# Kernel optimization log

Hardware: AMD Instinct MI355X
Metric: run time of the kernel (lower is better)

Reference implementation:

```python
import jax, jax.numpy as jnp
import numpy as np

B, N, D, DM, K = 2, 768, 32, 64, 16


def _linparams(key, cin, cout):
    kw, kb, ks, kt = jax.random.split(key, 4)
    W = jax.random.normal(kw, (cin, cout), jnp.float32) * np.float32(1.0 / np.sqrt(cin))
    b = 0.01 * jax.random.normal(kb, (cout,), jnp.float32)
    s = jax.random.uniform(ks, (cout,), jnp.float32, 0.5, 1.5)  # folded BN scale
    t = 0.1 * jax.random.normal(kt, (cout,), jnp.float32)       # folded BN shift
    return W, b, s, t


def setup_inputs():
    key = jax.random.key(0)
    kx, kh, k0, k1, k2, k3, k4 = jax.random.split(key, 7)
    inp = {
        'x': jax.random.normal(kx, (B, N, 3), jnp.float32),
        'h': jax.random.normal(kh, (B, N, D), jnp.float32),
    }
    specs = [('e0', 2 * D + 1, DM), ('e1', DM, DM), ('c0', DM, DM), ('c1', DM, 1), ('n0', D + DM, D)]
    for (name, cin, cout), k in zip(specs, [k0, k1, k2, k3, k4]):
        W, b, s, t = _linparams(k, cin, cout)
        inp[name + 'W'], inp[name + 'b'], inp[name + 's'], inp[name + 't'] = W, b, s, t
    return inp


def _layer(f, W, b, s, t):
    # 1x1 conv (= linear over last dim) + BN folded to per-channel affine + ReLU
    return jax.nn.relu((f @ W + b) * s + t)


def reference(x, h, e0W, e0b, e0s, e0t, e1W, e1b, e1s, e1t,
              c0W, c0b, c0s, c0t, c1W, c1b, c1s, c1t,
              n0W, n0b, n0s, n0t):
    Bn, Nn, Dn = h.shape
    # x_center[b,i,j] = x[b,j]; x_neighbor[b,i,j] = x[b,i]  => diff = x_j - x_i
    x_diff = x[:, None, :, :] - x[:, :, None, :]                   # (B,N,N,3)
    d2 = jnp.sum(x_diff * x_diff, axis=-1, keepdims=True)          # (B,N,N,1)
    h_c = jnp.broadcast_to(h[:, None, :, :], (Bn, Nn, Nn, Dn))     # h_center
    h_n = jnp.broadcast_to(h[:, :, None, :], (Bn, Nn, Nn, Dn))     # h_neighbor
    edge_feat = jnp.concatenate([h_c, h_n, d2], axis=-1)           # (B,N,N,2D+1)
    m_edge = _layer(_layer(edge_feat, e0W, e0b, e0s, e0t), e1W, e1b, e1s, e1t)  # (B,N,N,DM)
    w = _layer(_layer(m_edge, c0W, c0b, c0s, c0t), c1W, c1b, c1s, c1t)          # (B,N,N,1)
    x_update = x + jnp.sum(w * x_diff, axis=2)                     # (B,N,3)
    # knn gather: k nearest neighbors (incl. self) by squared distance
    idx = jax.lax.top_k(-d2[..., 0], K)[1]                         # (B,N,K)
    m_gathered = jnp.take_along_axis(m_edge, idx[..., None], axis=2)  # (B,N,K,DM)
    m_node = jnp.sum(m_gathered, axis=2)                           # (B,N,DM)
    node_feat = jnp.concatenate([h, m_node], axis=-1)              # (B,N,D+DM)
    h_update = _layer(node_feat, n0W, n0b, n0s, n0t)               # (B,N,D)
    return (x_update, h_update)
```

## Files before the change

### kernel.cpp

```cpp
#include <hip/hip_runtime.h>
#include <hip/hip_bf16.h>

#define Bn  2
#define Nn  768
#define Dh  32
#define DMm 64
#define KK  16
#define GI  3
#define TPRE 256
#define TMAIN 512
#define SAB 176

typedef __bf16 bf16x8 __attribute__((ext_vector_type(8)));
typedef float  f32x4  __attribute__((ext_vector_type(4)));


__global__ __launch_bounds__(TPRE) void egnn_pre(
    const float* __restrict__ X,  const float* __restrict__ H,
    const float* __restrict__ e0W, const float* __restrict__ e0b,
    const float* __restrict__ e0s, const float* __restrict__ e0t,
    const float* __restrict__ e1W, const float* __restrict__ e1b,
    const float* __restrict__ e1s, const float* __restrict__ e1t,
    const float* __restrict__ c0W, const float* __restrict__ c0b,
    const float* __restrict__ c0s, const float* __restrict__ c0t,
    const float* __restrict__ c1W, const float* __restrict__ c1b,
    const float* __restrict__ c1s, const float* __restrict__ c1t,
    const float* __restrict__ n0W, const float* __restrict__ n0b,
    const float* __restrict__ n0s, const float* __restrict__ n0t,
    __bf16* __restrict__ G1, float* __restrict__ G2,
    __bf16* __restrict__ W1f, __bf16* __restrict__ W2Tf,
    float* __restrict__ o1v, float* __restrict__ o2w3,
    float* __restrict__ Wnf, float* __restrict__ onOff,
    float* __restrict__ wd2, float* __restrict__ misc,
    int* __restrict__ knnIdx)
{
    const int tid = threadIdx.x;
    if (blockIdx.x < 384) {
        const int lane = tid & 63;
        const int row_i = blockIdx.x * 4 + (tid >> 6);
        const int b = row_i / Nn;
        const float xi0 = X[(size_t)row_i * 3 + 0];
        const float xi1 = X[(size_t)row_i * 3 + 1];
        const float xi2 = X[(size_t)row_i * 3 + 2];
        float v[Nn / 64];
        #pragma unroll
        for (int k = 0; k < Nn / 64; ++k) {
            int j = lane + (k << 6);
            size_t rj = (size_t)(b * Nn + j) * 3;
            float dx = X[rj + 0] - xi0;
            float dy = X[rj + 1] - xi1;
            float dz = X[rj + 2] - xi2;
            v[k] = __fadd_rn(__fadd_rn(__fmul_rn(dx, dx), __fmul_rn(dy, dy)),
                             __fmul_rn(dz, dz));
        }
        for (int r = 0; r < KK; ++r) {
            float bv = 3.4e38f; int bidx = Nn;
            #pragma unroll
            for (int k = 0; k < Nn / 64; ++k)
                if (v[k] < bv) { bv = v[k]; bidx = lane + (k << 6); }
            #pragma unroll
            for (int off = 32; off >= 1; off >>= 1) {
                float ov = __shfl_down(bv, off);
                int   oi = __shfl_down(bidx, off);
                if (ov < bv || (ov == bv && oi < bidx)) { bv = ov; bidx = oi; }
            }
            bidx = __shfl(bidx, 0);
            if (lane == 0) knnIdx[row_i * KK + r] = bidx;
            if ((bidx & 63) == lane) v[bidx >> 6] = 3.4e38f;
        }
    } else if (blockIdx.x < 432) {
        __shared__ float sWa[Dh * DMm], sWb[Dh * DMm], sOff[DMm], sH[32 * Dh];
        for (int k = tid; k < Dh * DMm; k += TPRE) {
            float s = e0s[k & 63];
            sWa[k] = e0W[k] * s;
            sWb[k] = e0W[Dh * DMm + k] * s;
        }
        if (tid < DMm) sOff[tid] = fmaf(e0b[tid], e0s[tid], e0t[tid]);
        const int row0 = (blockIdx.x - 384) * 32;
        for (int k = tid; k < 32 * Dh; k += TPRE) sH[k] = H[(size_t)row0 * Dh + k];
        __syncthreads();

        const int r = tid >> 3, g = tid & 7;
        float g1[8], g2[8];
        #pragma unroll
        for (int e = 0; e < 8; ++e) { g1[e] = 0.f; g2[e] = sOff[g * 8 + e]; }
        #pragma unroll
        for (int d = 0; d < Dh; ++d) {
            float hv = sH[r * Dh + d];
            #pragma unroll
            for (int e = 0; e < 8; ++e) {
                g1[e] = fmaf(hv, sWa[d * DMm + g * 8 + e], g1[e]);
                g2[e] = fmaf(hv, sWb[d * DMm + g * 8 + e], g2[e]);
            }
        }
        const size_t row = row0 + r;
        bf16x8 o;
        #pragma unroll
        for (int e = 0; e < 8; ++e) o[e] = (__bf16)g1[e];
        *(bf16x8*)(G1 + row * DMm + g * 8) = o;
        *(float4*)(G2 + row * DMm + g * 8)     = make_float4(g2[0], g2[1], g2[2], g2[3]);
        *(float4*)(G2 + row * DMm + g * 8 + 4) = make_float4(g2[4], g2[5], g2[6], g2[7]);
    } else {
        for (int src = tid; src < 4096; src += TPRE) {
            int k = src >> 6, n = src & 63;
            int fi = ((((k >> 5) * 4 + (n >> 4)) * 64) + ((k >> 3) & 3) * 16 + (n & 15)) * 8 + (k & 7);
            W1f[fi]  = (__bf16)(e1W[src] * e1s[n]);
            W2Tf[fi] = (__bf16)(c0W[src] * c0s[n]);
        }
        if (tid < DMm) {
            o1v[tid] = fmaf(e1b[tid], e1s[tid], e1t[tid]);
            wd2[tid] = e0W[64 * DMm + tid] * e0s[tid];
        }
        for (int u = tid; u < 1024; u += TPRE) {
            int lane = u >> 4, rem = u & 15, t4 = rem >> 2, r = rem & 3;
            int ch = t4 * 16 + (lane >> 4) * 4 + r;
            o2w3[2 * u]     = fmaf(c0b[ch], c0s[ch], c0t[ch]);
            o2w3[2 * u + 1] = c1W[ch] * c1s[0];
        }
        for (int idx = tid; idx < (Dh + DMm) * Dh; idx += TPRE)
            Wnf[idx] = n0W[idx] * n0s[idx & 31];
        if (tid < Dh) onOff[tid] = fmaf(n0b[tid], n0s[tid], n0t[tid]);
        if (tid == 0) misc[0] = fmaf(c1b[0], c1s[0], c1t[0]);
    }
}

__global__ __launch_bounds__(TMAIN, 2) void egnn_main(
    const float* __restrict__ X,  const float* __restrict__ H,
    const __bf16* __restrict__ G1, const float* __restrict__ G2,
    const __bf16* __restrict__ W1f, const __bf16* __restrict__ W2Tf,
    const float* __restrict__ o1v, const float* __restrict__ o2w3,
    const float* __restrict__ Wnf, const float* __restrict__ onOff,
    const float* __restrict__ wd2, const float* __restrict__ misc,
    const int* __restrict__ knnIdx,
    float* __restrict__ out)
{
    const int bid = blockIdx.x;
    const int b  = bid >> 8;
    const int i0 = (bid & 255) * GI;
    const int tid = threadIdx.x;
    const int wv = tid >> 6;
    const int lane = tid & 63;
    const int l15 = lane & 15;
    const int q   = lane >> 4;

    __shared__ float  sX[Nn * 3];
    __shared__ float  sD2[GI * Nn];
    __shared__ float  sWj[GI * Nn];
    __shared__ char   sHit[GI * Nn];
    __shared__ float  sMnode[GI * DMm];
    __shared__ float  sFeat[GI * 96];
    __shared__ float  sXacc[GI * 3];
    __shared__ __align__(16) char sA1[8][16 * SAB];

    for (int k = tid; k < Nn * 3; k += TMAIN) sX[k] = X[(size_t)b * Nn * 3 + k];
    for (int k = tid; k < GI * Nn / 4; k += TMAIN) ((int*)sHit)[k] = 0;
    if (tid < GI * DMm) sMnode[tid] = 0.f;
    if (tid < GI * Dh) {
        int i_l = tid >> 5, c = tid & 31;
        sFeat[i_l * 96 + c] = H[(size_t)(b * Nn + i0 + i_l) * Dh + c];
    }
    __syncthreads();

    #pragma unroll
    for (int i_l = 0; i_l < GI; ++i_l) {
        float xi0 = sX[(i0 + i_l) * 3 + 0];
        float xi1 = sX[(i0 + i_l) * 3 + 1];
        float xi2 = sX[(i0 + i_l) * 3 + 2];
        for (int j = tid; j < Nn; j += TMAIN) {
            float dx = sX[j * 3 + 0] - xi0;
            float dy = sX[j * 3 + 1] - xi1;
            float dz = sX[j * 3 + 2] - xi2;
            sD2[i_l * Nn + j] = __fadd_rn(__fadd_rn(__fmul_rn(dx, dx), __fmul_rn(dy, dy)),
                                          __fmul_rn(dz, dz));
        }
    }
    if (tid < GI * KK) {
        int i_l = tid >> 4, r = tid & 15;
        int idx = knnIdx[(size_t)(b * Nn + i0 + i_l) * KK + r];
        sHit[i_l * Nn + idx] = 1;
    }

    bf16x8 w1f[2][4], w2f[2][4];
    #pragma unroll
    for (int s = 0; s < 2; ++s)
        #pragma unroll
        for (int t4 = 0; t4 < 4; ++t4) {
            w1f[s][t4] = *(const bf16x8*)(W1f + (((s * 4 + t4) * 64 + lane) << 3));
            w2f[s][t4] = *(const bf16x8*)(W2Tf + (((s * 4 + t4) * 64 + lane) << 3));
        }
    float wd2c[2][8];
    #pragma unroll
    for (int s = 0; s < 2; ++s) {
        const float4* wp = (const float4*)(wd2 + s * 32 + q * 8);
        float4 wa = wp[0], wc = wp[1];
        wd2c[s][0] = wa.x; wd2c[s][1] = wa.y; wd2c[s][2] = wa.z; wd2c[s][3] = wa.w;
        wd2c[s][4] = wc.x; wd2c[s][5] = wc.y; wd2c[s][6] = wc.z; wd2c[s][7] = wc.w;
    }
    float o1c[4];
    #pragma unroll
    for (int t4 = 0; t4 < 4; ++t4) o1c[t4] = o1v[t4 * 16 + l15];
    float4 o2w3q[8];
    #pragma unroll
    for (int u = 0; u < 8; ++u) o2w3q[u] = ((const float4*)o2w3)[lane * 8 + u];
    const float c1off = misc[0];
    __syncthreads();

    for (int i_l = 0; i_l < GI; ++i_l) {
        const int ig = i0 + i_l;
        float g2c[2][8];
        #pragma unroll
        for (int s = 0; s < 2; ++s) {
            const float4* gp = (const float4*)(G2 + (size_t)(b * Nn + ig) * DMm + s * 32 + q * 8);
            float4 ga = gp[0], gc = gp[1];
            g2c[s][0] = ga.x; g2c[s][1] = ga.y; g2c[s][2] = ga.z; g2c[s][3] = ga.w;
            g2c[s][4] = gc.x; g2c[s][5] = gc.y; g2c[s][6] = gc.z; g2c[s][7] = gc.w;
        }
        for (int t = wv; t < 48; t += 8) {
            const int base = t * 16;
            const int jm = base + l15;

            float d2v = sD2[i_l * Nn + jm];

            bf16x8 a0f[2];
            #pragma unroll
            for (int s = 0; s < 2; ++s) {
                bf16x8 g1v = *(const bf16x8*)(G1 + (size_t)(b * Nn + jm) * DMm + s * 32 + q * 8);
                bf16x8 af;
                #pragma unroll
                for (int e = 0; e < 8; ++e) {
                    float v = fmaf(d2v, wd2c[s][e], g2c[s][e]) + (float)g1v[e];
                    af[e] = (__bf16)fmaxf(v, 0.f);
                }
                a0f[s] = af;
            }

            f32x4 acc[4];
            #pragma unroll
            for (int t4 = 0; t4 < 4; ++t4) acc[t4] = f32x4{0.f, 0.f, 0.f, 0.f};
            #pragma unroll
            for (int s = 0; s < 2; ++s)
                #pragma unroll
                for (int t4 = 0; t4 < 4; ++t4)
                    acc[t4] = __builtin_amdgcn_mfma_f32_16x16x32_bf16(a0f[s], w1f[s][t4], acc[t4], 0, 0, 0);
            #pragma unroll
            for (int t4 = 0; t4 < 4; ++t4)
                #pragma unroll
                for (int r = 0; r < 4; ++r) {
                    float v = fmaxf(acc[t4][r] + o1c[t4], 0.f);
                    acc[t4][r] = v;
                    *(__bf16*)&sA1[wv][(q * 4 + r) * SAB + (t4 * 16 + l15) * 2] = (__bf16)v;
                }
            {
                unsigned hw = *(const unsigned*)&sHit[i_l * Nn + base + q * 4];
                if (hw) {
                    #pragma unroll
                    for (int r = 0; r < 4; ++r)
                        if ((hw >> (8 * r)) & 0xff) {
                            #pragma unroll
                            for (int t4 = 0; t4 < 4; ++t4)
                                atomicAdd(&sMnode[i_l * DMm + t4 * 16 + l15], acc[t4][r]);
                        }
                }
            }
            bf16x8 a1f[2];
            #pragma unroll
            for (int s = 0; s < 2; ++s)
                a1f[s] = *(const bf16x8*)&sA1[wv][l15 * SAB + s * 64 + q * 16];

            f32x4 acc2[4];
            #pragma unroll
            for (int t4 = 0; t4 < 4; ++t4) acc2[t4] = f32x4{0.f, 0.f, 0.f, 0.f};
            #pragma unroll
            for (int s = 0; s < 2; ++s)
                #pragma unroll
                for (int t4 = 0; t4 < 4; ++t4)
                    acc2[t4] = __builtin_amdgcn_mfma_f32_16x16x32_bf16(w2f[s][t4], a1f[s], acc2[t4], 0, 0, 0);
            float p = 0.f;
            #pragma unroll
            for (int t4 = 0; t4 < 4; ++t4)
                #pragma unroll
                for (int r = 0; r < 4; ++r) {
                    int u = t4 * 4 + r;
                    float4 qv = o2w3q[u >> 1];
                    float o2 = (u & 1) ? qv.z : qv.x;
                    float w3 = (u & 1) ? qv.w : qv.y;
                    p = fmaf(fmaxf(acc2[t4][r] + o2, 0.f), w3, p);
                }
            p += __shfl_xor(p, 16);
            p += __shfl_xor(p, 32);
            if (lane < 16) sWj[i_l * Nn + base + l15] = fmaxf(p + c1off, 0.f);
        }
    }
    __syncthreads();

    if (wv < GI) {
        const int i_l = wv;
        float xi0 = sX[(i0 + i_l) * 3 + 0];
        float xi1 = sX[(i0 + i_l) * 3 + 1];
        float xi2 = sX[(i0 + i_l) * 3 + 2];
        float xa0 = 0.f, xa1 = 0.f, xa2 = 0.f;
        #pragma unroll
        for (int k = 0; k < Nn / 64; ++k) {
            int j = lane + (k << 6);
            float w = sWj[i_l * Nn + j];
            xa0 = fmaf(w, sX[j * 3 + 0] - xi0, xa0);
            xa1 = fmaf(w, sX[j * 3 + 1] - xi1, xa1);
            xa2 = fmaf(w, sX[j * 3 + 2] - xi2, xa2);
        }
        #pragma unroll
        for (int off = 32; off >= 1; off >>= 1) {
            xa0 += __shfl_down(xa0, off);
            xa1 += __shfl_down(xa1, off);
            xa2 += __shfl_down(xa2, off);
        }
        if (lane == 0) {
            sXacc[i_l * 3 + 0] = xa0;
            sXacc[i_l * 3 + 1] = xa1;
            sXacc[i_l * 3 + 2] = xa2;
        }
    }
    if (tid < GI * DMm) {
        int i_l = tid >> 6, ch = tid & 63;
        sFeat[i_l * 96 + Dh + ch] = sMnode[tid];
    }
    __syncthreads();

    if (tid < GI * Dh) {
        int i_l = tid >> 5, oc = tid & 31;
        float z = onOff[oc];
        #pragma unroll
        for (int c = 0; c < Dh + DMm; ++c)
            z = fmaf(sFeat[i_l * 96 + c], Wnf[c * Dh + oc], z);
        out[(size_t)Bn * Nn * 3 + (size_t)(b * Nn + i0 + i_l) * Dh + oc] = fmaxf(z, 0.f);
    }
    if (tid < GI * 3) {
        int i_l = tid / 3, c = tid - i_l * 3;
        out[(size_t)(b * Nn + i0 + i_l) * 3 + c] = sX[(i0 + i_l) * 3 + c] + sXacc[i_l * 3 + c];
    }
}

extern "C" void kernel_launch(void* const* d_in, const int* in_sizes, int n_in,
                              void* d_out, int out_size, void* d_ws, size_t ws_size,
                              hipStream_t stream) {
    const float* X   = (const float*)d_in[0];
    const float* H   = (const float*)d_in[1];
    const float* e0W = (const float*)d_in[2];
    const float* e0b = (const float*)d_in[3];
    const float* e0s = (const float*)d_in[4];
    const float* e0t = (const float*)d_in[5];
    const float* e1W = (const float*)d_in[6];
    const float* e1b = (const float*)d_in[7];
    const float* e1s = (const float*)d_in[8];
    const float* e1t = (const float*)d_in[9];
    const float* c0W = (const float*)d_in[10];
    const float* c0b = (const float*)d_in[11];
    const float* c0s = (const float*)d_in[12];
    const float* c0t = (const float*)d_in[13];
    const float* c1W = (const float*)d_in[14];
    const float* c1b = (const float*)d_in[15];
    const float* c1s = (const float*)d_in[16];
    const float* c1t = (const float*)d_in[17];
    const float* n0W = (const float*)d_in[18];
    const float* n0b = (const float*)d_in[19];
    const float* n0s = (const float*)d_in[20];
    const float* n0t = (const float*)d_in[21];
    float* out = (float*)d_out;

    char* ws = (char*)d_ws;
    __bf16* G1    = (__bf16*)(ws);
    float*  G2    = (float*)(ws + 196608);
    __bf16* W1f   = (__bf16*)(ws + 589824);
    __bf16* W2Tf  = (__bf16*)(ws + 598016);
    float*  o1v   = (float*)(ws + 606208);
    float*  o2w3  = (float*)(ws + 606464);
    float*  Wnf   = (float*)(ws + 614656);
    float*  onOff = (float*)(ws + 626944);
    float*  wd2   = (float*)(ws + 627072);
    float*  misc  = (float*)(ws + 627328);
    int*    knnIdx= (int*)(ws + 627456);

    egnn_pre<<<dim3(433), dim3(TPRE), 0, stream>>>(X, H,
        e0W, e0b, e0s, e0t, e1W, e1b, e1s, e1t,
        c0W, c0b, c0s, c0t, c1W, c1b, c1s, c1t,
        n0W, n0b, n0s, n0t,
        G1, G2, W1f, W2Tf, o1v, o2w3, Wnf, onOff, wd2, misc, knnIdx);
    egnn_main<<<dim3(Bn * Nn / GI), dim3(TMAIN), 0, stream>>>(X, H,
        G1, G2, W1f, W2Tf, o1v, o2w3, Wnf, onOff, wd2, misc, knnIdx, out);
}
```

Baseline: 162.7 us.

## Keep first MLP output in registers by transposing MFMA and permuting W2 layout

The first edge-MLP MFMA is transposed so its accumulator layout directly forms the B operand of the second MFMA. W2 is pre-permuted in the prep kernel to match, which removes the per-wave LDS staging buffer (sA1) and its round trip. The bias is folded into the accumulator init, and the knn hit flag moves into the sign bit of the d2 value, dropping the separate sHit array. d2 weights and G2 are held as bf16 to save registers, which adds conversions and slightly lowers precision.

Result: faster. 155.3 us (-4.5%).

```diff
diff --git a/kernel.cpp b/kernel.cpp
--- a/kernel.cpp
+++ b/kernel.cpp
@@ -9,7 +9,6 @@
 #define GI  3
 #define TPRE 256
 #define TMAIN 512
-#define SAB 176
 
 typedef __bf16 bf16x8 __attribute__((ext_vector_type(8)));
 typedef float  f32x4  __attribute__((ext_vector_type(4)));
@@ -32,7 +31,7 @@
     float* __restrict__ o1v, float* __restrict__ o2w3,
     float* __restrict__ Wnf, float* __restrict__ onOff,
     float* __restrict__ wd2, float* __restrict__ misc,
-    int* __restrict__ knnIdx)
+    int* __restrict__ knnIdx, float* __restrict__ o1p)
 {
     const int tid = threadIdx.x;
     if (blockIdx.x < 384) {
@@ -103,13 +102,21 @@
     } else {
         for (int src = tid; src < 4096; src += TPRE) {
             int k = src >> 6, n = src & 63;
-            int fi = ((((k >> 5) * 4 + (n >> 4)) * 64) + ((k >> 3) & 3) * 16 + (n & 15)) * 8 + (k & 7);
-            W1f[fi]  = (__bf16)(e1W[src] * e1s[n]);
-            W2Tf[fi] = (__bf16)(c0W[src] * c0s[n]);
+            int fi1 = ((((k >> 5) * 4 + (n >> 4)) * 64) + ((k >> 3) & 3) * 16 + (n & 15)) * 8 + (k & 7);
+            W1f[fi1] = (__bf16)(e1W[src] * e1s[n]);
+            int ch1 = k, ch2 = n;
+            int s2 = ch1 >> 5, u2 = (ch1 >> 4) & 1, q2 = (ch1 >> 2) & 3, r2 = ch1 & 3;
+            int fi2 = (((s2 * 4 + (ch2 >> 4)) * 64) + q2 * 16 + (ch2 & 15)) * 8 + (u2 * 4 + r2);
+            W2Tf[fi2] = (__bf16)(c0W[src] * c0s[ch2]);
         }
         if (tid < DMm) {
             o1v[tid] = fmaf(e1b[tid], e1s[tid], e1t[tid]);
             wd2[tid] = e0W[64 * DMm + tid] * e0s[tid];
+        }
+        for (int u = tid; u < 1024; u += TPRE) {
+            int lane = u >> 4, t4 = (u >> 2) & 3, r = u & 3;
+            int ch = t4 * 16 + ((lane >> 4) & 3) * 4 + r;
+            o1p[u] = fmaf(e1b[ch], e1s[ch], e1t[ch]);
         }
         for (int u = tid; u < 1024; u += TPRE) {
             int lane = u >> 4, rem = u & 15, t4 = rem >> 2, r = rem & 3;
@@ -128,7 +135,7 @@
     const float* __restrict__ X,  const float* __restrict__ H,
     const __bf16* __restrict__ G1, const float* __restrict__ G2,
     const __bf16* __restrict__ W1f, const __bf16* __restrict__ W2Tf,
-    const float* __restrict__ o1v, const float* __restrict__ o2w3,
+    const float* __restrict__ o1p, const float* __restrict__ o2w3,
     const float* __restrict__ Wnf, const float* __restrict__ onOff,
     const float* __restrict__ wd2, const float* __restrict__ misc,
     const int* __restrict__ knnIdx,
@@ -146,14 +153,11 @@
     __shared__ float  sX[Nn * 3];
     __shared__ float  sD2[GI * Nn];
     __shared__ float  sWj[GI * Nn];
-    __shared__ char   sHit[GI * Nn];
     __shared__ float  sMnode[GI * DMm];
     __shared__ float  sFeat[GI * 96];
     __shared__ float  sXacc[GI * 3];
-    __shared__ __align__(16) char sA1[8][16 * SAB];
 
     for (int k = tid; k < Nn * 3; k += TMAIN) sX[k] = X[(size_t)b * Nn * 3 + k];
-    for (int k = tid; k < GI * Nn / 4; k += TMAIN) ((int*)sHit)[k] = 0;
     if (tid < GI * DMm) sMnode[tid] = 0.f;
     if (tid < GI * Dh) {
         int i_l = tid >> 5, c = tid & 31;
@@ -174,10 +178,11 @@
                                           __fmul_rn(dz, dz));
         }
     }
+    __syncthreads();
     if (tid < GI * KK) {
         int i_l = tid >> 4, r = tid & 15;
         int idx = knnIdx[(size_t)(b * Nn + i0 + i_l) * KK + r];
-        sHit[i_l * Nn + idx] = 1;
+        ((unsigned*)sD2)[i_l * Nn + idx] |= 0x80000000u;
     }
 
     bf16x8 w1f[2][4], w2f[2][4];
@@ -188,17 +193,21 @@
             w1f[s][t4] = *(const bf16x8*)(W1f + (((s * 4 + t4) * 64 + lane) << 3));
             w2f[s][t4] = *(const bf16x8*)(W2Tf + (((s * 4 + t4) * 64 + lane) << 3));
         }
-    float wd2c[2][8];
+    bf16x8 wd2b[2];
     #pragma unroll
     for (int s = 0; s < 2; ++s) {
         const float4* wp = (const float4*)(wd2 + s * 32 + q * 8);
         float4 wa = wp[0], wc = wp[1];
-        wd2c[s][0] = wa.x; wd2c[s][1] = wa.y; wd2c[s][2] = wa.z; wd2c[s][3] = wa.w;
-        wd2c[s][4] = wc.x; wd2c[s][5] = wc.y; wd2c[s][6] = wc.z; wd2c[s][7] = wc.w;
-    }
-    float o1c[4];
+        float t[8] = {wa.x, wa.y, wa.z, wa.w, wc.x, wc.y, wc.z, wc.w};
+        bf16x8 o;
+        #pragma unroll
+        for (int e = 0; e < 8; ++e) o[e] = (__bf16)t[e];
+        wd2b[s] = o;
+    }
+    f32x4 o1q[4];
     #pragma unroll
-    for (int t4 = 0; t4 < 4; ++t4) o1c[t4] = o1v[t4 * 16 + l15];
+    for (int t4 = 0; t4 < 4; ++t4)
+        o1q[t4] = *(const f32x4*)(o1p + lane * 16 + t4 * 4);
     float4 o2w3q[8];
     #pragma unroll
     for (int u = 0; u < 8; ++u) o2w3q[u] = ((const float4*)o2w3)[lane * 8 + u];
@@ -207,19 +216,24 @@
 
     for (int i_l = 0; i_l < GI; ++i_l) {
         const int ig = i0 + i_l;
-        float g2c[2][8];
+        bf16x8 g2b[2];
         #pragma unroll
         for (int s = 0; s < 2; ++s) {
             const float4* gp = (const float4*)(G2 + (size_t)(b * Nn + ig) * DMm + s * 32 + q * 8);
             float4 ga = gp[0], gc = gp[1];
-            g2c[s][0] = ga.x; g2c[s][1] = ga.y; g2c[s][2] = ga.z; g2c[s][3] = ga.w;
-            g2c[s][4] = gc.x; g2c[s][5] = gc.y; g2c[s][6] = gc.z; g2c[s][7] = gc.w;
+            float t[8] = {ga.x, ga.y, ga.z, ga.w, gc.x, gc.y, gc.z, gc.w};
+            bf16x8 o;
+            #pragma unroll
+            for (int e = 0; e < 8; ++e) o[e] = (__bf16)t[e];
+            g2b[s] = o;
         }
         for (int t = wv; t < 48; t += 8) {
             const int base = t * 16;
             const int jm = base + l15;
 
-            float d2v = sD2[i_l * Nn + jm];
+            unsigned du = __float_as_uint(sD2[i_l * Nn + jm]);
+            float d2v = __uint_as_float(du & 0x7fffffffu);
+            bool hit = (du >> 31) != 0;
 
             bf16x8 a0f[2];
             #pragma unroll
@@ -228,53 +242,54 @@
                 bf16x8 af;
                 #pragma unroll
                 for (int e = 0; e < 8; ++e) {
-                    float v = fmaf(d2v, wd2c[s][e], g2c[s][e]) + (float)g1v[e];
+                    float v = fmaf(d2v, (float)wd2b[s][e], (float)g2b[s][e]) + (float)g1v[e];
                     af[e] = (__bf16)fmaxf(v, 0.f);
                 }
                 a0f[s] = af;
             }
 
-            f32x4 acc[4];
-            #pragma unroll
-            for (int t4 = 0; t4 < 4; ++t4) acc[t4] = f32x4{0.f, 0.f, 0.f, 0.f};
+            f32x4 acc1[4];
+            #pragma unroll
+            for (int t4 = 0; t4 < 4; ++t4) acc1[t4] = o1q[t4];
             #pragma unroll
             for (int s = 0; s < 2; ++s)
                 #pragma unroll
                 for (int t4 = 0; t4 < 4; ++t4)
-                    acc[t4] = __builtin_amdgcn_mfma_f32_16x16x32_bf16(a0f[s], w1f[s][t4], acc[t4], 0, 0, 0);
+                    acc1[t4] = __builtin_amdgcn_mfma_f32_16x16x32_bf16(w1f[s][t4], a0f[s], acc1[t4], 0, 0, 0);
             #pragma unroll
             for (int t4 = 0; t4 < 4; ++t4)
                 #pragma unroll
-                for (int r = 0; r < 4; ++r) {
-                    float v = fmaxf(acc[t4][r] + o1c[t4], 0.f);
-                    acc[t4][r] = v;
-                    *(__bf16*)&sA1[wv][(q * 4 + r) * SAB + (t4 * 16 + l15) * 2] = (__bf16)v;
-                }
-            {
-                unsigned hw = *(const unsigned*)&sHit[i_l * Nn + base + q * 4];
-                if (hw) {
+                for (int r = 0; r < 4; ++r)
+                    acc1[t4][r] = fmaxf(acc1[t4][r], 0.f);
+
+            if (hit) {
+                #pragma unroll
+                for (int t4 = 0; t4 < 4; ++t4)
                     #pragma unroll
                     for (int r = 0; r < 4; ++r)
-                        if ((hw >> (8 * r)) & 0xff) {
-                            #pragma unroll
-                            for (int t4 = 0; t4 < 4; ++t4)
-                                atomicAdd(&sMnode[i_l * DMm + t4 * 16 + l15], acc[t4][r]);
-                        }
-                }
+                        atomicAdd(&sMnode[i_l * DMm + t4 * 16 + q * 4 + r], acc1[t4][r]);
             }
-            bf16x8 a1f[2];
+
+            bf16x8 bfr[2];
+            #pragma unroll
+            for (int s = 0; s < 2; ++s) {
+                bf16x8 o;
+                #pragma unroll
+                for (int u = 0; u < 2; ++u)
+                    #pragma unroll
+                    for (int r = 0; r < 4; ++r)
+                        o[u * 4 + r] = (__bf16)acc1[2 * s + u][r];
+                bfr[s] = o;
+            }
+
+            f32x4 acc2[4];
+            #pragma unroll
+            for (int t4 = 0; t4 < 4; ++t4) acc2[t4] = f32x4{0.f, 0.f, 0.f, 0.f};
             #pragma unroll
             for (int s = 0; s < 2; ++s)
-                a1f[s] = *(const bf16x8*)&sA1[wv][l15 * SAB + s * 64 + q * 16];
-
-            f32x4 acc2[4];
-            #pragma unroll
-            for (int t4 = 0; t4 < 4; ++t4) acc2[t4] = f32x4{0.f, 0.f, 0.f, 0.f};
-            #pragma unroll
-            for (int s = 0; s < 2; ++s)
                 #pragma unroll
                 for (int t4 = 0; t4 < 4; ++t4)
-                    acc2[t4] = __builtin_amdgcn_mfma_f32_16x16x32_bf16(w2f[s][t4], a1f[s], acc2[t4], 0, 0, 0);
+                    acc2[t4] = __builtin_amdgcn_mfma_f32_16x16x32_bf16(w2f[s][t4], bfr[s], acc2[t4], 0, 0, 0);
             float p = 0.f;
             #pragma unroll
             for (int t4 = 0; t4 < 4; ++t4)
@@ -378,12 +393,13 @@
     float*  wd2   = (float*)(ws + 627072);
     float*  misc  = (float*)(ws + 627328);
     int*    knnIdx= (int*)(ws + 627456);
+    float*  o1p   = (float*)(ws + 725760);
 
     egnn_pre<<<dim3(433), dim3(TPRE), 0, stream>>>(X, H,
         e0W, e0b, e0s, e0t, e1W, e1b, e1s, e1t,
         c0W, c0b, c0s, c0t, c1W, c1b, c1s, c1t,
         n0W, n0b, n0s, n0t,
-        G1, G2, W1f, W2Tf, o1v, o2w3, Wnf, onOff, wd2, misc, knnIdx);
+        G1, G2, W1f, W2Tf, o1v, o2w3, Wnf, onOff, wd2, misc, knnIdx, o1p);
     egnn_main<<<dim3(Bn * Nn / GI), dim3(TMAIN), 0, stream>>>(X, H,
-        G1, G2, W1f, W2Tf, o1v, o2w3, Wnf, onOff, wd2, misc, knnIdx, out);
+        G1, G2, W1f, W2Tf, o1p, o2w3, Wnf, onOff, wd2, misc, knnIdx, out);
 }
```
